# Kernel optimization log

Hardware: AMD Instinct MI355X
Metric: run time of the kernel (lower is better)

Reference implementation:

```python
import jax, jax.numpy as jnp
import numpy as np

S, B, E, H = 2048, 4, 512, 8
HD = E // H


def setup_inputs() -> dict:
    key = jax.random.key(0)
    ks = jax.random.split(key, 5)
    scale = 1.0 / np.sqrt(E)
    return {
        "query": jax.random.normal(ks[0], (S, B, E), jnp.float32),
        "key": jax.random.normal(ks[1], (S, B, E), jnp.float32),
        "value": jax.random.normal(ks[2], (S, B, E), jnp.float32),
        "in_proj_weight": jax.random.normal(ks[3], (3 * E, E), jnp.float32) * scale,
        "in_proj_bias": jnp.zeros((3 * E,), jnp.float32),
        "out_proj_weight": jax.random.normal(ks[4], (E, E), jnp.float32) * scale,
        "out_proj_bias": jnp.zeros((E,), jnp.float32),
    }


def reference(query, key, value, in_proj_weight, in_proj_bias, out_proj_weight, out_proj_bias):
    tgt_len, bsz, embed_dim = query.shape
    src_len = key.shape[0]
    # Quirk of this module: first chunk (w_qk) projects BOTH q and k; third chunk projects v.
    w_qk = in_proj_weight[:embed_dim]
    w_v = in_proj_weight[2 * embed_dim:]
    b_qk = in_proj_bias[:embed_dim]
    b_v = in_proj_bias[2 * embed_dim:]
    q = query @ w_qk.T + b_qk          # [S, B, E]
    k = key @ w_qk.T + b_qk
    v = value @ w_v.T + b_v
    # (S, B, E) -> (B*H, S, HD)
    def split_heads(x, n):
        return x.reshape(n, bsz * H, HD).transpose(1, 0, 2)
    q = split_heads(q, tgt_len) / jnp.sqrt(jnp.asarray(HD, q.dtype))
    k = split_heads(k, src_len)
    v = split_heads(v, src_len)
    scores = jnp.einsum("bqd,bkd->bqk", q, k)          # [B*H, S, S] full score matrix
    attn = jax.nn.softmax(scores, axis=-1)
    out = jnp.einsum("bqk,bkd->bqd", attn, v)          # [B*H, S, HD]
    out = out.transpose(1, 0, 2).reshape(tgt_len * bsz, embed_dim)
    out = out @ out_proj_weight.T + out_proj_bias
    return out.reshape(tgt_len, bsz, embed_dim)
```

## Files before the change

kernel.cpp:

```cpp
#include <hip/hip_runtime.h>
#include <hip/hip_bf16.h>

typedef __attribute__((ext_vector_type(8))) short s16x8;
typedef __attribute__((ext_vector_type(4))) short s16x4;
typedef __attribute__((ext_vector_type(4))) float f32x4;

#if __has_builtin(__builtin_amdgcn_exp2f)
#define EXP2F(x) __builtin_amdgcn_exp2f(x)
#else
#define EXP2F(x) exp2f(x)
#endif

#define EMB   512
#define MROWS 8192

__device__ __forceinline__ short f2bf(float f) {
    union { float f; unsigned u; } z; z.f = f;
    unsigned r = z.u + 0x7FFF + ((z.u >> 16) & 1);
    return (short)(r >> 16);
}
__device__ __forceinline__ short f2bf_fast(float f) {
    union { float f; unsigned u; } z; z.f = f;
    return (short)((z.u + 0x8000u) >> 16);
}
__device__ __forceinline__ short f2bf_cvt(float f) {
    union { __hip_bfloat16 h; short s; } cv;
    cv.h = __float2bfloat16(f);
    return cv.s;
}
__device__ __forceinline__ int swzs(int s) { return s ^ ((s >> 3) & 7); }

__device__ __forceinline__ void barrier_fast() {
    asm volatile("s_waitcnt lgkmcnt(0)" ::: "memory");
    __builtin_amdgcn_s_barrier();
    __builtin_amdgcn_sched_barrier(0);
}

__global__ __launch_bounds__(256) void w_to_bf16(const float* __restrict__ W,
                                                 short* __restrict__ wb, int n)
{
    int i = (blockIdx.x * 256 + threadIdx.x) * 8;
    if (i < n) {
        f32x4 a = *(const f32x4*)(W + i);
        f32x4 b = *(const f32x4*)(W + i + 4);
        s16x8 o;
        o[0] = f2bf(a[0]); o[1] = f2bf(a[1]); o[2] = f2bf(a[2]); o[3] = f2bf(a[3]);
        o[4] = f2bf(b[0]); o[5] = f2bf(b[1]); o[6] = f2bf(b[2]); o[7] = f2bf(b[3]);
        *(s16x8*)(wb + i) = o;
    }
}

template<int AF32, int BF32>
__device__ __forceinline__ void gemm_mainloop(const void* __restrict__ Ag,
                                              const void* __restrict__ Bg,
                                              short* sA, short* sB,
                                              f32x4 acc[2][4], int ld, int Klen)
{
    const int tid  = threadIdx.x;
    const int lane = tid & 63;
    const int wv   = tid >> 6;
    const int lsw  = lane ^ ((lane >> 3) & 7);
    const int amt  = (wv >> 1) * 2;
    const int bnt  = (wv & 1) * 4;

    const int srow = tid >> 3, qd = tid & 7;
    const int offL = (qd >> 2) * 4096
                   + swzs((srow >> 4) * 64 + (qd & 3) * 16 + (srow & 15)) * 8;
    const int offH = (qd >> 2) * 4096
                   + swzs(((srow >> 4) + 4) * 64 + (qd & 3) * 16 + (srow & 15)) * 8;

    f32x4 aF0[4], aF1[4], bF0[4], bF1[4];
    s16x8 aH0[2], aH1[2], bH0[2], bH1[2];

    auto loadX = [&](const void* G, int kt, f32x4 fr[4], s16x8 hr[2], int F32) {
        if (F32) {
            const float* g = (const float*)G + (size_t)srow * ld + kt + qd * 8;
            fr[0] = *(const f32x4*)g;
            fr[1] = *(const f32x4*)(g + 4);
            fr[2] = *(const f32x4*)(g + (size_t)64 * ld);
            fr[3] = *(const f32x4*)(g + (size_t)64 * ld + 4);
        } else {
            const short* g = (const short*)G + (size_t)srow * ld + kt + qd * 8;
            hr[0] = *(const s16x8*)g;
            hr[1] = *(const s16x8*)(g + (size_t)64 * ld);
        }
    };
    auto commitX = [&](short* s, f32x4 fr[4], s16x8 hr[2], int F32) {
        if (F32) {
            s16x8 o;
            o[0] = f2bf_fast(fr[0][0]); o[1] = f2bf_fast(fr[0][1]);
            o[2] = f2bf_fast(fr[0][2]); o[3] = f2bf_fast(fr[0][3]);
            o[4] = f2bf_fast(fr[1][0]); o[5] = f2bf_fast(fr[1][1]);
            o[6] = f2bf_fast(fr[1][2]); o[7] = f2bf_fast(fr[1][3]);
            *(s16x8*)(s + offL) = o;
            o[0] = f2bf_fast(fr[2][0]); o[1] = f2bf_fast(fr[2][1]);
            o[2] = f2bf_fast(fr[2][2]); o[3] = f2bf_fast(fr[2][3]);
            o[4] = f2bf_fast(fr[3][0]); o[5] = f2bf_fast(fr[3][1]);
            o[6] = f2bf_fast(fr[3][2]); o[7] = f2bf_fast(fr[3][3]);
            *(s16x8*)(s + offH) = o;
        } else {
            *(s16x8*)(s + offL) = hr[0];
            *(s16x8*)(s + offH) = hr[1];
        }
    };
    auto compute = [&](const short* sAc, const short* sBc) {
#pragma unroll
        for (int h = 0; h < 2; ++h) {
            s16x8 a[2], b[4];
#pragma unroll
            for (int i = 0; i < 2; ++i)
                a[i] = *(const s16x8*)(sAc + h * 4096 + ((amt + i) * 64 + lsw) * 8);
#pragma unroll
            for (int j = 0; j < 4; ++j)
                b[j] = *(const s16x8*)(sBc + h * 4096 + ((bnt + j) * 64 + lsw) * 8);
#pragma unroll
            for (int i = 0; i < 2; ++i)
#pragma unroll
                for (int j = 0; j < 4; ++j)
                    acc[i][j] = __builtin_amdgcn_mfma_f32_16x16x32_bf16(a[i], b[j], acc[i][j], 0, 0, 0);
        }
    };

    loadX(Ag, 0, aF0, aH0, AF32);  loadX(Bg, 0, bF0, bH0, BF32);
    loadX(Ag, 64, aF1, aH1, AF32); loadX(Bg, 64, bF1, bH1, BF32);
    commitX(sA, aF0, aH0, AF32); commitX(sB, bF0, bH0, BF32);
    barrier_fast();

    for (int kt = 0; kt < Klen; kt += 128) {
        const int k2 = (kt + 128 < Klen) ? kt + 128 : 0;
        loadX(Ag, k2, aF0, aH0, AF32); loadX(Bg, k2, bF0, bH0, BF32);
        compute(sA, sB);
        commitX(sA + 8192, aF1, aH1, AF32); commitX(sB + 8192, bF1, bH1, BF32);
        barrier_fast();
        const int k3 = (kt + 192 < Klen) ? kt + 192 : 0;
        loadX(Ag, k3, aF1, aH1, AF32); loadX(Bg, k3, bF1, bH1, BF32);
        compute(sA + 8192, sB + 8192);
        commitX(sA, aF0, aH0, AF32); commitX(sB, bF0, bH0, BF32);
        barrier_fast();
    }
}

__global__ __launch_bounds__(512, 4) void qkv_proj(const float* __restrict__ query,
                                                   const float* __restrict__ key,
                                                   const float* __restrict__ value,
                                                   const short* __restrict__ wb,
                                                   const float* __restrict__ bias,
                                                   short* __restrict__ q,
                                                   short* __restrict__ k,
                                                   short* __restrict__ vt)
{
    __shared__ __align__(16) short smem[32768];
    short* sA = smem;
    short* sB = smem + 16384;

    const int z = blockIdx.z;
    const float* X  = (z == 0) ? query : (z == 1) ? key : value;
    const short* Wz = wb   + (z == 2 ? (size_t)1024 * EMB : 0);
    const float* bz = bias + (z == 2 ? 1024 : 0);
    const float scale = (z == 0) ? 0.125f * 1.44269504f : 1.0f;

    const int blockM = blockIdx.x * 128, blockN = blockIdx.y * 128;

    f32x4 acc[2][4];
#pragma unroll
    for (int i = 0; i < 2; ++i)
#pragma unroll
        for (int j = 0; j < 4; ++j)
            acc[i][j] = (f32x4){0.f, 0.f, 0.f, 0.f};

    gemm_mainloop<1, 0>(X + (size_t)blockM * EMB, Wz + (size_t)blockN * EMB,
                        sA, sB, acc, EMB, EMB);

    const int tid = threadIdx.x, lane = tid & 63, wv = tid >> 6;
    const int l15 = lane & 15, quad = lane >> 4;
    const int wm = (wv >> 1) * 32, wn = (wv & 1) * 64;

#pragma unroll
    for (int j = 0; j < 4; ++j) {
        int colL = wn + j * 16 + l15;
        float bval = bz[blockN + colL];
        int hL = colL >> 6, hd = colL & 63;
#pragma unroll
        for (int i = 0; i < 2; ++i) {
#pragma unroll
            for (int r = 0; r < 4; ++r) {
                int rowL = wm + i * 16 + quad * 4 + r;
                int b = rowL & 3, sp = rowL >> 2;
                float val = (acc[i][j][r] + bval) * scale;
                int idx;
                if (z == 2) {
                    int R = (b * 2 + hL) * 64 + hd;
                    idx = R * 32 + (((sp >> 3) ^ (R & 3)) << 3) + (sp & 7);
                } else {
                    idx = ((b * 2 + hL) * 32 + sp) * 64 + hd;
                }
                smem[idx] = f2bf(val);
            }
        }
    }
    barrier_fast();

    if (z == 2) {
        int R = tid;
        int b = tid >> 7, hL = (tid >> 6) & 1, hd = tid & 63;
        int h = (blockN >> 6) + hL;
        short* dst = vt + ((size_t)(b * 8 + h) * 64 + hd) * 2048 + (blockM >> 2);
#pragma unroll
        for (int u = 0; u < 4; ++u)
            ((s16x8*)dst)[u] = *(const s16x8*)(smem + R * 32 + ((u ^ (R & 3)) << 3));
    } else {
        const s16x8* src = (const s16x8*)(smem + tid * 32);
        int b = tid >> 7, hL = (tid >> 6) & 1;
        int sp = (tid >> 1) & 31, hdh = (tid & 1) * 32;
        int h = (blockN >> 6) + hL;
        short* dstp = (z == 0) ? q : k;
        short* dst = dstp + ((size_t)(b * 8 + h) * 2048 + (blockM >> 2) + sp) * 64 + hdh;
#pragma unroll
        for (int u = 0; u < 4; ++u) ((s16x8*)dst)[u] = src[u];
    }
}

__global__ __launch_bounds__(512, 2) void flash_attn(const short* __restrict__ q,
                                                     const short* __restrict__ k,
                                                     const short* __restrict__ vt,
                                                     short* __restrict__ attn)
{
    __shared__ __align__(16) short sK[2][8192];
    __shared__ __align__(16) short sV[2][8192];
    const int bh = blockIdx.x;
    const int q0 = blockIdx.y * 256;
    const int tid = threadIdx.x, wv = tid >> 6, lane = tid & 63;
    const int l15 = lane & 15, quad = lane >> 4;
    const int lsw = lane ^ ((lane >> 3) & 7);

    s16x8 qf[2][2];
#pragma unroll
    for (int qr = 0; qr < 2; ++qr) {
        const short* qp = q + ((size_t)(bh * 2048 + q0 + wv * 32 + qr * 16 + l15)) * 64 + quad * 8;
        qf[qr][0] = *(const s16x8*)qp;
        qf[qr][1] = *(const s16x8*)(qp + 32);
    }

    const short* kg = k  + (size_t)bh * 2048 * 64;
    const short* vg = vt + (size_t)bh * 64 * 2048;

    const int tL = tid & 255, sub = tid >> 8;
    const int rk = tL >> 2, qd = tL & 3;
    const int pr = (rk & 35) | ((rk & 24) >> 1) | ((rk & 4) << 2);
    const int kw0 = sub * 4096 + swzs((pr >> 4) * 64 + qd * 16 + (pr & 15)) * 8;
    const int vw0 = sub * 4096 + swzs((rk >> 4) * 64 + qd * 16 + (rk & 15)) * 8;
    const short* kgt = kg + (size_t)(sub * 64 + rk) * 64 + qd * 8;
    const short* vgt = vg + (size_t)rk * 2048 + sub * 64 + qd * 8;

    f32x4 o[2][4];
    float ls[2][4];
#pragma unroll
    for (int qr = 0; qr < 2; ++qr)
#pragma unroll
        for (int i = 0; i < 4; ++i) { o[qr][i] = (f32x4){0.f, 0.f, 0.f, 0.f}; ls[qr][i] = 0.f; }

    s16x8 kA, kB, vA, vB;
    auto loadT = [&](int kt) {
        kA = *(const s16x8*)(kgt + (size_t)kt * 64);
        kB = *(const s16x8*)(kgt + (size_t)kt * 64 + 32);
        vA = *(const s16x8*)(vgt + kt);
        vB = *(const s16x8*)(vgt + kt + 32);
    };
    auto commitT = [&](int buf) {
        *(s16x8*)(sK[buf] + kw0)        = kA;
        *(s16x8*)(sK[buf] + kw0 + 2048) = kB;
        *(s16x8*)(sV[buf] + vw0)        = vA;
        *(s16x8*)(sV[buf] + vw0 + 2048) = vB;
    };
    auto computeQK = [&](const short* Kc, f32x4 sc[2][4]) {
#pragma unroll
        for (int ct = 0; ct < 4; ++ct) {
            s16x8 kf0 = *(const s16x8*)(Kc + (ct * 64 + lsw) * 8);
            s16x8 kf1 = *(const s16x8*)(Kc + (ct * 64 + lsw) * 8 + 2048);
#pragma unroll
            for (int qr = 0; qr < 2; ++qr) {
                f32x4 c = (f32x4){0.f, 0.f, 0.f, 0.f};
                c = __builtin_amdgcn_mfma_f32_16x16x32_bf16(kf0, qf[qr][0], c, 0, 0, 0);
                c = __builtin_amdgcn_mfma_f32_16x16x32_bf16(kf1, qf[qr][1], c, 0, 0, 0);
                sc[qr][ct] = c;
            }
        }
    };
    auto softmaxPV = [&](f32x4 sc[2][4], const short* Vc) {
        s16x8 pf[2][2];
#pragma unroll
        for (int qr = 0; qr < 2; ++qr)
#pragma unroll
            for (int c = 0; c < 2; ++c)
#pragma unroll
                for (int h = 0; h < 2; ++h)
#pragma unroll
                    for (int r = 0; r < 4; ++r) {
                        float p = EXP2F(sc[qr][2 * c + h][r]);
                        ls[qr][r] += p;
                        pf[qr][c][h * 4 + r] = f2bf_cvt(p);
                    }
#pragma unroll
        for (int nt = 0; nt < 4; ++nt)
#pragma unroll
            for (int c = 0; c < 2; ++c) {
                s16x8 vf = *(const s16x8*)(Vc + ((c * 4 + nt) * 64 + lsw) * 8);
#pragma unroll
                for (int qr = 0; qr < 2; ++qr)
                    o[qr][nt] = __builtin_amdgcn_mfma_f32_16x16x32_bf16(pf[qr][c], vf, o[qr][nt], 0, 0, 0);
            }
    };

    loadT(0);
    commitT(0);
    __syncthreads();

    int cur = 0;
    for (int kt = 0; kt < 2048; kt += 128) {
        loadT((kt + 128) & 2047);

        f32x4 sc0[2][4], sc1[2][4];
        computeQK(sK[cur], sc0);
        computeQK(sK[cur] + 4096, sc1);
        softmaxPV(sc0, sV[cur]);
        softmaxPV(sc1, sV[cur] + 4096);

        commitT(cur ^ 1);
        __syncthreads();
        cur ^= 1;
    }

    const int b = bh >> 3, h = bh & 7;
#pragma unroll
    for (int qr = 0; qr < 2; ++qr) {
        float s = ls[qr][0] + ls[qr][1] + ls[qr][2] + ls[qr][3];
        s += __shfl_xor(s, 16, 64);
        s += __shfl_xor(s, 32, 64);
        float sinv = 1.0f / s;
        float inv[4];
#pragma unroll
        for (int r = 0; r < 4; ++r)
            inv[r] = __shfl(sinv, quad * 20 + r, 64);
#pragma unroll
        for (int r = 0; r < 4; ++r) {
            int srow = q0 + wv * 32 + qr * 16 + quad * 4 + r;
#pragma unroll
            for (int nt = 0; nt < 4; ++nt)
                attn[(size_t)(srow * 4 + b) * 512 + h * 64 + nt * 16 + l15] = f2bf(o[qr][nt][r] * inv[r]);
        }
    }
}

__global__ __launch_bounds__(512, 4) void out_proj(const short* __restrict__ attn,
                                                   const float* __restrict__ W,
                                                   const float* __restrict__ bias,
                                                   float* __restrict__ out)
{
    __shared__ __align__(16) short smem[32768];
    short* sA = smem;
    short* sB = smem + 16384;
    const int blockM = blockIdx.x * 128, blockN = blockIdx.y * 128;

    f32x4 acc[2][4];
#pragma unroll
    for (int i = 0; i < 2; ++i)
#pragma unroll
        for (int j = 0; j < 4; ++j)
            acc[i][j] = (f32x4){0.f, 0.f, 0.f, 0.f};

    gemm_mainloop<0, 1>(attn + (size_t)blockM * EMB, W + (size_t)blockN * EMB,
                        sA, sB, acc, EMB, EMB);

    const int tid = threadIdx.x, lane = tid & 63, wv = tid >> 6;
    const int l15 = lane & 15, quad = lane >> 4;
    const int wm = (wv >> 1) * 32, wn = (wv & 1) * 64;

#pragma unroll
    for (int j = 0; j < 4; ++j) {
        int col = blockN + wn + j * 16 + l15;
        float bval = bias[col];
#pragma unroll
        for (int i = 0; i < 2; ++i) {
#pragma unroll
            for (int r = 0; r < 4; ++r) {
                int row = blockM + wm + i * 16 + quad * 4 + r;
                out[(size_t)row * 512 + col] = acc[i][j][r] + bval;
            }
        }
    }
}

extern "C" void kernel_launch(void* const* d_in, const int* in_sizes, int n_in,
                              void* d_out, int out_size, void* d_ws, size_t ws_size,
                              hipStream_t stream)
{
    const float* query = (const float*)d_in[0];
    const float* key   = (const float*)d_in[1];
    const float* value = (const float*)d_in[2];
    const float* ipw   = (const float*)d_in[3];
    const float* ipb   = (const float*)d_in[4];
    const float* opw   = (const float*)d_in[5];
    const float* opb   = (const float*)d_in[6];
    float* out = (float*)d_out;

    const size_t NELEM = (size_t)MROWS * EMB;
    short* q    = (short*)d_ws;
    short* k    = q + NELEM;
    short* attn = k + NELEM;
    short* vt   = (short*)d_out;
    short* wb   = (short*)d_out + NELEM;

    w_to_bf16 <<<dim3(384),      256, 0, stream>>>(ipw, wb, 1536 * EMB);
    qkv_proj  <<<dim3(64, 4, 3), 512, 0, stream>>>(query, key, value, wb, ipb, q, k, vt);
    flash_attn<<<dim3(32, 8),    512, 0, stream>>>(q, k, vt, attn);
    out_proj  <<<dim3(64, 4),    512, 0, stream>>>(attn, opw, opb, out);
}
```

Before: 174.1 us.

## Load bf16 GEMM operand directly into LDS via global_load_lds

In the shared projection GEMM mainloop, the operand that is already bf16 (weights in qkv_proj, attention output in out_proj) is now loaded straight from global memory into LDS with global_load_lds. This replaces the register round-trip and explicit LDS store, and uses a new LDS layout with a vmcnt-based barrier. The goal is fewer VGPRs and fewer load/store instructions in the projection kernels. The risk is in the vmcnt(4) wait count and buffer ordering, and the projections are only part of the total time.

Measured after the change: 181.6 us. +4.3%, slower.

```diff
diff --git a/kernel.cpp b/kernel.cpp
--- a/kernel.cpp
+++ b/kernel.cpp
@@ -34,6 +34,17 @@
     asm volatile("s_waitcnt lgkmcnt(0)" ::: "memory");
     __builtin_amdgcn_s_barrier();
     __builtin_amdgcn_sched_barrier(0);
+}
+__device__ __forceinline__ void barrier_gld() {
+    asm volatile("s_waitcnt vmcnt(4) lgkmcnt(0)" ::: "memory");
+    __builtin_amdgcn_s_barrier();
+    __builtin_amdgcn_sched_barrier(0);
+}
+
+__device__ __forceinline__ void gld16(const short* src, short* dst) {
+    __builtin_amdgcn_global_load_lds(
+        (const __attribute__((address_space(1))) void*)src,
+        (__attribute__((address_space(3))) void*)dst, 16, 0, 0);
 }
 
 __global__ __launch_bounds__(256) void w_to_bf16(const float* __restrict__ W,
@@ -50,7 +61,7 @@
     }
 }
 
-template<int AF32, int BF32>
+template<int AGLD>
 __device__ __forceinline__ void gemm_mainloop(const void* __restrict__ Ag,
                                               const void* __restrict__ Bg,
                                               short* sA, short* sB,
@@ -63,56 +74,72 @@
     const int amt  = (wv >> 1) * 2;
     const int bnt  = (wv & 1) * 4;
 
+    const float* rG = (const float*)(AGLD ? Bg : Ag);
+    const short* gG = (const short*)(AGLD ? Ag : Bg);
+    short* sR = AGLD ? sB : sA;
+    short* sG = AGLD ? sA : sB;
+
     const int srow = tid >> 3, qd = tid & 7;
     const int offL = (qd >> 2) * 4096
                    + swzs((srow >> 4) * 64 + (qd & 3) * 16 + (srow & 15)) * 8;
     const int offH = (qd >> 2) * 4096
                    + swzs(((srow >> 4) + 4) * 64 + (qd & 3) * 16 + (srow & 15)) * 8;
 
-    f32x4 aF0[4], aF1[4], bF0[4], bF1[4];
-    s16x8 aH0[2], aH1[2], bH0[2], bH1[2];
-
-    auto loadX = [&](const void* G, int kt, f32x4 fr[4], s16x8 hr[2], int F32) {
-        if (F32) {
-            const float* g = (const float*)G + (size_t)srow * ld + kt + qd * 8;
-            fr[0] = *(const f32x4*)g;
-            fr[1] = *(const f32x4*)(g + 4);
-            fr[2] = *(const f32x4*)(g + (size_t)64 * ld);
-            fr[3] = *(const f32x4*)(g + (size_t)64 * ld + 4);
-        } else {
-            const short* g = (const short*)G + (size_t)srow * ld + kt + qd * 8;
-            hr[0] = *(const s16x8*)g;
-            hr[1] = *(const s16x8*)(g + (size_t)64 * ld);
-        }
-    };
-    auto commitX = [&](short* s, f32x4 fr[4], s16x8 hr[2], int F32) {
-        if (F32) {
-            s16x8 o;
-            o[0] = f2bf_fast(fr[0][0]); o[1] = f2bf_fast(fr[0][1]);
-            o[2] = f2bf_fast(fr[0][2]); o[3] = f2bf_fast(fr[0][3]);
-            o[4] = f2bf_fast(fr[1][0]); o[5] = f2bf_fast(fr[1][1]);
-            o[6] = f2bf_fast(fr[1][2]); o[7] = f2bf_fast(fr[1][3]);
-            *(s16x8*)(s + offL) = o;
-            o[0] = f2bf_fast(fr[2][0]); o[1] = f2bf_fast(fr[2][1]);
-            o[2] = f2bf_fast(fr[2][2]); o[3] = f2bf_fast(fr[2][3]);
-            o[4] = f2bf_fast(fr[3][0]); o[5] = f2bf_fast(fr[3][1]);
-            o[6] = f2bf_fast(fr[3][2]); o[7] = f2bf_fast(fr[3][3]);
-            *(s16x8*)(s + offH) = o;
-        } else {
-            *(s16x8*)(s + offL) = hr[0];
-            *(s16x8*)(s + offH) = hr[1];
-        }
-    };
-    auto compute = [&](const short* sAc, const short* sBc) {
+    const int c0 = wv * 2, c1 = wv * 2 + 1;
+    const short* gsrc0 = gG + (size_t)((c0 & 7) * 16 + (lane & 15)) * ld
+                       + (c0 >> 3) * 32 + (lane >> 4) * 8;
+    const short* gsrc1 = gG + (size_t)((c1 & 7) * 16 + (lane & 15)) * ld
+                       + (c1 >> 3) * 32 + (lane >> 4) * 8;
+    const int gdst0 = (c0 >> 3) * 4096 + (c0 & 7) * 512;
+    const int gdst1 = (c1 >> 3) * 4096 + (c1 & 7) * 512;
+
+    f32x4 F0[4], F1[4];
+
+    auto loadR = [&](int kt, f32x4 fr[4]) {
+        const float* g = rG + (size_t)srow * ld + kt + qd * 8;
+        fr[0] = *(const f32x4*)g;
+        fr[1] = *(const f32x4*)(g + 4);
+        fr[2] = *(const f32x4*)(g + (size_t)64 * ld);
+        fr[3] = *(const f32x4*)(g + (size_t)64 * ld + 4);
+    };
+    auto commitR = [&](short* s, f32x4 fr[4]) {
+        s16x8 o;
+        o[0] = f2bf_fast(fr[0][0]); o[1] = f2bf_fast(fr[0][1]);
+        o[2] = f2bf_fast(fr[0][2]); o[3] = f2bf_fast(fr[0][3]);
+        o[4] = f2bf_fast(fr[1][0]); o[5] = f2bf_fast(fr[1][1]);
+        o[6] = f2bf_fast(fr[1][2]); o[7] = f2bf_fast(fr[1][3]);
+        *(s16x8*)(s + offL) = o;
+        o[0] = f2bf_fast(fr[2][0]); o[1] = f2bf_fast(fr[2][1]);
+        o[2] = f2bf_fast(fr[2][2]); o[3] = f2bf_fast(fr[2][3]);
+        o[4] = f2bf_fast(fr[3][0]); o[5] = f2bf_fast(fr[3][1]);
+        o[6] = f2bf_fast(fr[3][2]); o[7] = f2bf_fast(fr[3][3]);
+        *(s16x8*)(s + offH) = o;
+    };
+    auto gldT = [&](int kt, int buf) {
+        gld16(gsrc0 + kt, sG + buf * 8192 + gdst0);
+        gld16(gsrc1 + kt, sG + buf * 8192 + gdst1);
+    };
+    auto compute = [&](int buf) {
+        const short* sRc = sR + buf * 8192;
+        const short* sGc = sG + buf * 8192;
 #pragma unroll
         for (int h = 0; h < 2; ++h) {
             s16x8 a[2], b[4];
-#pragma unroll
-            for (int i = 0; i < 2; ++i)
-                a[i] = *(const s16x8*)(sAc + h * 4096 + ((amt + i) * 64 + lsw) * 8);
-#pragma unroll
-            for (int j = 0; j < 4; ++j)
-                b[j] = *(const s16x8*)(sBc + h * 4096 + ((bnt + j) * 64 + lsw) * 8);
+            if (AGLD) {
+#pragma unroll
+                for (int i = 0; i < 2; ++i)
+                    a[i] = *(const s16x8*)(sGc + h * 4096 + (amt + i) * 512 + lane * 8);
+#pragma unroll
+                for (int j = 0; j < 4; ++j)
+                    b[j] = *(const s16x8*)(sRc + h * 4096 + ((bnt + j) * 64 + lsw) * 8);
+            } else {
+#pragma unroll
+                for (int i = 0; i < 2; ++i)
+                    a[i] = *(const s16x8*)(sRc + h * 4096 + ((amt + i) * 64 + lsw) * 8);
+#pragma unroll
+                for (int j = 0; j < 4; ++j)
+                    b[j] = *(const s16x8*)(sGc + h * 4096 + (bnt + j) * 512 + lane * 8);
+            }
 #pragma unroll
             for (int i = 0; i < 2; ++i)
 #pragma unroll
@@ -121,22 +148,25 @@
         }
     };
 
-    loadX(Ag, 0, aF0, aH0, AF32);  loadX(Bg, 0, bF0, bH0, BF32);
-    loadX(Ag, 64, aF1, aH1, AF32); loadX(Bg, 64, bF1, bH1, BF32);
-    commitX(sA, aF0, aH0, AF32); commitX(sB, bF0, bH0, BF32);
-    barrier_fast();
+    gldT(0, 0);
+    loadR(0, F0);
+    loadR(64, F1);
+    commitR(sR, F0);
+    barrier_gld();
 
     for (int kt = 0; kt < Klen; kt += 128) {
         const int k2 = (kt + 128 < Klen) ? kt + 128 : 0;
-        loadX(Ag, k2, aF0, aH0, AF32); loadX(Bg, k2, bF0, bH0, BF32);
-        compute(sA, sB);
-        commitX(sA + 8192, aF1, aH1, AF32); commitX(sB + 8192, bF1, bH1, BF32);
-        barrier_fast();
+        gldT((kt + 64 < Klen) ? kt + 64 : 0, 1);
+        loadR(k2, F0);
+        compute(0);
+        commitR(sR + 8192, F1);
+        barrier_gld();
         const int k3 = (kt + 192 < Klen) ? kt + 192 : 0;
-        loadX(Ag, k3, aF1, aH1, AF32); loadX(Bg, k3, bF1, bH1, BF32);
-        compute(sA + 8192, sB + 8192);
-        commitX(sA, aF0, aH0, AF32); commitX(sB, bF0, bH0, BF32);
-        barrier_fast();
+        gldT(k2, 0);
+        loadR(k3, F1);
+        compute(1);
+        commitR(sR, F0);
+        barrier_gld();
     }
 }
 
@@ -168,8 +198,8 @@
         for (int j = 0; j < 4; ++j)
             acc[i][j] = (f32x4){0.f, 0.f, 0.f, 0.f};
 
-    gemm_mainloop<1, 0>(X + (size_t)blockM * EMB, Wz + (size_t)blockN * EMB,
-                        sA, sB, acc, EMB, EMB);
+    gemm_mainloop<0>(X + (size_t)blockM * EMB, Wz + (size_t)blockN * EMB,
+                     sA, sB, acc, EMB, EMB);
 
     const int tid = threadIdx.x, lane = tid & 63, wv = tid >> 6;
     const int l15 = lane & 15, quad = lane >> 4;
@@ -368,8 +398,8 @@
         for (int j = 0; j < 4; ++j)
             acc[i][j] = (f32x4){0.f, 0.f, 0.f, 0.f};
 
-    gemm_mainloop<0, 1>(attn + (size_t)blockM * EMB, W + (size_t)blockN * EMB,
-                        sA, sB, acc, EMB, EMB);
+    gemm_mainloop<1>(attn + (size_t)blockM * EMB, W + (size_t)blockN * EMB,
+                     sA, sB, acc, EMB, EMB);
 
     const int tid = threadIdx.x, lane = tid & 63, wv = tid >> 6;
     const int l15 = lane & 15, quad = lane >> 4;
```
